# Kernel optimization log

Hardware: AMD Instinct MI355X
Metric: run time of the kernel (lower is better)

## Reference

```python
import jax, jax.numpy as jnp
import numpy as np
from jax import lax

NUM_DISP = 64
BLOCK = 21
EPS = 1e-12  # F.normalize default eps


def _box_sum(v):
    # v: (N, H, W) -> BLOCK x BLOCK zero-padded box sum (same shape), separable.
    p = BLOCK // 2
    v = v[:, None]  # (N,1,H,W)
    kv = jnp.ones((1, 1, BLOCK, 1), v.dtype)
    kh = jnp.ones((1, 1, 1, BLOCK), v.dtype)
    v = lax.conv_general_dilated(v, kv, (1, 1), ((p, p), (0, 0)))
    v = lax.conv_general_dilated(v, kh, (1, 1), ((0, 0), (p, p)))
    return v[:, 0]


def _l2norm_c(img):
    n = jnp.sqrt(jnp.sum(img * img, axis=1, keepdims=True))
    return img / jnp.maximum(n, EPS)


def _disparity(left, right):
    # left, right: (B, 3, H, W)
    left = _l2norm_c(left)
    right = _l2norm_c(right)
    B, C, H, W = left.shape
    d = jnp.arange(NUM_DISP)
    xs = jnp.arange(W)
    idx = xs[None, :] - d[:, None]              # (D, W): source column in right image
    valid = (idx >= 0)
    r_shift = right[:, :, :, jnp.clip(idx, 0)]  # (B, C, H, D, W)
    r_shift = jnp.where(valid[None, None, None], r_shift, 0.0)
    # per-pixel channel-summed absolute difference -> (B, D, H, W)
    diff = jnp.sum(jnp.abs(left[:, :, :, None, :] - r_shift), axis=1)  # (B, H, D, W)
    diff = jnp.transpose(diff, (0, 2, 1, 3))    # (B, D, H, W)
    cost = _box_sum(diff.reshape(B * NUM_DISP, H, W)).reshape(B, NUM_DISP, H, W)
    cost = cost / (C * BLOCK * BLOCK)           # mean SAD over block elements
    return jnp.argmin(cost, axis=1).astype(left.dtype)  # (B, H, W)


def setup_inputs() -> dict:
    key = jax.random.key(0)
    k1, k2 = jax.random.split(key)
    x = jax.random.normal(k1, (2, 6, 320, 512), dtype=jnp.float32)
    gt = jax.random.normal(k2, (2, 6, 320, 512), dtype=jnp.float32)
    return {"x": x, "gt": gt}


def reference(x, gt):
    disp_gt = _disparity(gt[:, :3], gt[:, 3:])
    disp_pred = _disparity(x[:, :3], x[:, 3:])
    return jnp.mean(jnp.abs(disp_pred - disp_gt))
```

## Files before the change

### kernel.cpp

```cpp
#include <hip/hip_runtime.h>
#include <math.h>

constexpr int B = 2, H = 320, W = 512, D = 64;
constexpr int HW = H * W;
constexpr int R = 10;
constexpr int SEG = 80;
constexpr int NSEG = H / SEG;
constexpr int RS = 548;
constexpr int QUADS = B * HW / 4;
constexpr float EPS = 1e-12f;
constexpr unsigned KM = 0xFFFFFFC0u;

__global__ void k_norm(const float* __restrict__ x, const float* __restrict__ gt,
                       float4* __restrict__ nrm4) {
    int idx = blockIdx.x * 128 + threadIdx.x;
    if (idx >= 2 * B * (HW / 4)) return;
    int t = idx / (B * (HW / 4));
    int rem = idx - t * (B * (HW / 4));
    int b = rem / (HW / 4);
    int hw4 = rem - b * (HW / 4);
    const float* p = (t == 0 ? x : gt) + (size_t)b * 6 * HW + 4 * hw4;
    float4 c[6];
#pragma unroll
    for (int ch = 0; ch < 6; ++ch) c[ch] = *(const float4*)(p + (size_t)ch * HW);
    float4* q = nrm4 + (size_t)(t * B + b) * 2 * HW + 4 * hw4;
    float4 o0[4], o1[4];
    const float* cf = (const float*)c;
#pragma unroll
    for (int k = 0; k < 4; ++k) {
        float v0 = cf[k], v1 = cf[4 + k], v2 = cf[8 + k];
        float v3 = cf[12 + k], v4 = cf[16 + k], v5 = cf[20 + k];
        float n1 = fmaxf(sqrtf(v0 * v0 + v1 * v1 + v2 * v2), EPS);
        float n2 = fmaxf(sqrtf(v3 * v3 + v4 * v4 + v5 * v5), EPS);
        o0[k] = make_float4(v0 / n1, v1 / n1, v2 / n1, 0.f);
        o1[k] = make_float4(v3 / n2, v4 / n2, v5 / n2, 0.f);
    }
#pragma unroll
    for (int k = 0; k < 4; ++k) { q[k] = o0[k]; q[HW + k] = o1[k]; }
}

template<bool FUSE>
__global__ __launch_bounds__(512, 2) void k_cost(const float4* __restrict__ nrm4,
                                                 float* __restrict__ cost,
                                                 const float* __restrict__ cprev,
                                                 float* __restrict__ dprev, int t) {
    const int blk = blockIdx.x;
    const int combo = blk & 7;
    const int d = blk >> 3;
    const int b = combo >> 2;
    const int seg = combo & 3;
    const int w = threadIdx.x;
    const float4* L4 = nrm4 + (size_t)(t * B + b) * 2 * HW;
    const float4* R4 = L4 + HW;
    const bool val = (w >= d);
    const int wr = val ? (w - d) : 0;
    const int h0 = seg * SEG;

    __shared__ float ring[21][W];
    __shared__ float vsb[2][8][RS];
    {
        int j = w >> 6, k = w & 63;
        if (k < 10)      { vsb[0][j][k] = 0.f;       vsb[1][j][k] = 0.f; }
        else if (k < 20) { vsb[0][j][512 + k] = 0.f; vsb[1][j][512 + k] = 0.f; }
    }

    auto diff = [&](int h) -> float {
        float4 l = L4[(size_t)h * W + w];
        if (val) {
            float4 r = R4[(size_t)h * W + wr];
            return fabsf(l.x - r.x) + fabsf(l.y - r.y) + fabsf(l.z - r.z);
        }
        return fabsf(l.x) + fabsf(l.y) + fabsf(l.z);
    };

    float vs = 0.f;
    for (int k = 0; k < 20; ++k) {
        int h = h0 - R + k;
        float dv0 = (h >= 0) ? diff(h) : 0.f;
        ring[k][w] = dv0;
        vs += dv0;
    }
    ring[20][w] = 0.f;

    const float* cp0 = nullptr; const float* cp1 = nullptr;
    int px0 = 0, px1 = 0;
    float best0 = 3.4e38f, best1 = 3.4e38f;
    int bd0 = 0, bd1 = 0;
    if (FUSE) {
        px0 = blk * 640 + w;
        int b0 = (px0 >= HW) ? 1 : 0;
        cp0 = cprev + (size_t)b0 * D * HW + (px0 - b0 * HW);
        if (w < 128) {
            px1 = blk * 640 + 512 + w;
            int b1 = (px1 >= HW) ? 1 : 0;
            cp1 = cprev + (size_t)b1 * D * HW + (px1 - b1 * HW);
        }
    }

    const int cc = threadIdx.x >> 3;
    const int jj = threadIdx.x & 7;
    float* cp = cost + ((size_t)(b * D + d) * H) * W;

    float dvv[8];
#pragma unroll
    for (int j = 0; j < 8; ++j) {
        int hn = h0 + j + R;
        dvv[j] = (hn < H) ? diff(hn) : 0.f;
    }

    int slot0 = 20;
    int dc = 0;
    for (int ss = 0; ss < 10; ++ss) {
        const int nd = (ss < 4) ? 7 : 6;
        int sl[8];
        float dold[8];
#pragma unroll
        for (int j = 0; j < 8; ++j) { int s2 = slot0 + j; if (s2 >= 21) s2 -= 21; sl[j] = s2; }
#pragma unroll
        for (int j = 0; j < 8; ++j) dold[j] = ring[sl[j]][w];
        float fv0[7], fv1[7];
        if (FUSE) {
#pragma unroll
            for (int q = 0; q < 7; ++q)
                if (q < nd) fv0[q] = cp0[(size_t)(dc + q) * HW];
            if (w < 128) {
#pragma unroll
                for (int q = 0; q < 7; ++q)
                    if (q < nd) fv1[q] = cp1[(size_t)(dc + q) * HW];
            }
        }
#pragma unroll
        for (int j = 0; j < 8; ++j) ring[sl[j]][w] = dvv[j];
        float* vrow = &vsb[ss & 1][0][0];
#pragma unroll
        for (int j = 0; j < 8; ++j) { vs += dvv[j] - dold[j]; vrow[j * RS + 10 + w] = vs; }
        float dvn[8];
        if (ss < 9) {
#pragma unroll
            for (int j = 0; j < 8; ++j) {
                int hn = h0 + (ss + 1) * 8 + j + R;
                dvn[j] = (hn < H) ? diff(hn) : 0.f;
            }
        } else {
#pragma unroll
            for (int j = 0; j < 8; ++j) dvn[j] = 0.f;
        }
        __syncthreads();
        const float* vp = &vsb[ss & 1][jj][8 * cc];
        float wnd[28];
#pragma unroll
        for (int q = 0; q < 7; ++q) {
            float4 v4 = *(const float4*)(vp + 4 * q);
            wnd[4 * q] = v4.x; wnd[4 * q + 1] = v4.y;
            wnd[4 * q + 2] = v4.z; wnd[4 * q + 3] = v4.w;
        }
        float o = 0.f;
#pragma unroll
        for (int k = 0; k < 21; ++k) o += wnd[k];
        float out[8];
        out[0] = o;
#pragma unroll
        for (int k = 1; k < 8; ++k) { o += wnd[20 + k] - wnd[k - 1]; out[k] = o; }
        float* op = cp + (size_t)(h0 + ss * 8 + jj) * W + 8 * cc;
        *(float4*)(op)     = make_float4(out[0], out[1], out[2], out[3]);
        *(float4*)(op + 4) = make_float4(out[4], out[5], out[6], out[7]);
        if (FUSE) {
#pragma unroll
            for (int q = 0; q < 7; ++q)
                if (q < nd && fv0[q] < best0) { best0 = fv0[q]; bd0 = dc + q; }
            if (w < 128) {
#pragma unroll
                for (int q = 0; q < 7; ++q)
                    if (q < nd && fv1[q] < best1) { best1 = fv1[q]; bd1 = dc + q; }
            }
        }
#pragma unroll
        for (int j = 0; j < 8; ++j) dvv[j] = dvn[j];
        dc += nd;
        slot0 += 8; if (slot0 >= 21) slot0 -= 21;
    }
    if (FUSE) {
        dprev[px0] = (float)bd0;
        if (w < 128) dprev[px1] = (float)bd1;
    }
}

__global__ void k_aminA(const float* __restrict__ cost, uint4* __restrict__ keys) {
    int idx = blockIdx.x * 256 + threadIdx.x;
    int c = idx / QUADS;
    int q = idx - c * QUADS;
    int b = q / (QUADS / B);
    int ql = q - b * (QUADS / B);
    const float* cp = cost + (size_t)b * D * HW + 4 * ql;
    int d0 = c * 16;
    float4 v = *(const float4*)(cp + (size_t)d0 * HW);
    unsigned kx = (__float_as_uint(v.x) & KM) | (unsigned)d0;
    unsigned ky = (__float_as_uint(v.y) & KM) | (unsigned)d0;
    unsigned kz = (__float_as_uint(v.z) & KM) | (unsigned)d0;
    unsigned kw = (__float_as_uint(v.w) & KM) | (unsigned)d0;
#pragma unroll 4
    for (int k = 1; k < 16; ++k) {
        unsigned d = (unsigned)(d0 + k);
        v = *(const float4*)(cp + (size_t)(d0 + k) * HW);
        unsigned e;
        e = (__float_as_uint(v.x) & KM) | d; kx = (e < kx) ? e : kx;
        e = (__float_as_uint(v.y) & KM) | d; ky = (e < ky) ? e : ky;
        e = (__float_as_uint(v.z) & KM) | d; kz = (e < kz) ? e : kz;
        e = (__float_as_uint(v.w) & KM) | d; kw = (e < kw) ? e : kw;
    }
    keys[idx] = make_uint4(kx, ky, kz, kw);
}

__global__ void k_aminB(const uint4* __restrict__ keys, const float* __restrict__ disp0,
                        float* __restrict__ part) {
    int q = blockIdx.x * 256 + threadIdx.x;
    uint4 m = keys[q];
#pragma unroll
    for (int c = 1; c < 4; ++c) {
        uint4 kc = keys[(size_t)c * QUADS + q];
        m.x = (kc.x < m.x) ? kc.x : m.x;
        m.y = (kc.y < m.y) ? kc.y : m.y;
        m.z = (kc.z < m.z) ? kc.z : m.z;
        m.w = (kc.w < m.w) ? kc.w : m.w;
    }
    float4 d0 = *(const float4*)(disp0 + (size_t)4 * q);
    float s = fabsf((float)(m.x & 63u) - d0.x) + fabsf((float)(m.y & 63u) - d0.y) +
              fabsf((float)(m.z & 63u) - d0.z) + fabsf((float)(m.w & 63u) - d0.w);
    __shared__ float sm[256];
    sm[threadIdx.x] = s;
    __syncthreads();
    for (int off = 128; off; off >>= 1) {
        if (threadIdx.x < off) sm[threadIdx.x] += sm[threadIdx.x + off];
        __syncthreads();
    }
    if (!threadIdx.x) part[blockIdx.x] = sm[0];
}

__global__ void k_amin(const float* __restrict__ cost, float* __restrict__ disp) {
    int blk = blockIdx.x;
    int b = (blk * 1024 >= HW) ? 1 : 0;
    int hw0 = blk * 1024 - b * HW + threadIdx.x * 4;
    const float* cp = cost + (size_t)b * D * HW + hw0;
    float4 v = *(const float4*)cp;
    float bb[4] = {v.x, v.y, v.z, v.w};
    int bd[4] = {0, 0, 0, 0};
    for (int d = 1; d < D; ++d) {
        v = *(const float4*)(cp + (size_t)d * HW);
        if (v.x < bb[0]) { bb[0] = v.x; bd[0] = d; }
        if (v.y < bb[1]) { bb[1] = v.y; bd[1] = d; }
        if (v.z < bb[2]) { bb[2] = v.z; bd[2] = d; }
        if (v.w < bb[3]) { bb[3] = v.w; bd[3] = d; }
    }
    *(float4*)(disp + (size_t)blk * 1024 + threadIdx.x * 4) =
        make_float4((float)bd[0], (float)bd[1], (float)bd[2], (float)bd[3]);
}

__global__ void k_red2(const float* __restrict__ part, float* __restrict__ out,
                       int nb, float inv) {
    __shared__ float sm[256];
    int tid = threadIdx.x;
    float s = 0.f;
    for (int i = tid; i < nb; i += 256) s += part[i];
    sm[tid] = s;
    __syncthreads();
    for (int off = 128; off; off >>= 1) {
        if (tid < off) sm[tid] += sm[tid + off];
        __syncthreads();
    }
    if (!tid) out[0] = sm[0] * inv;
}

extern "C" void kernel_launch(void* const* d_in, const int* in_sizes, int n_in,
                              void* d_out, int out_size, void* d_ws, size_t ws_size,
                              hipStream_t stream) {
    const float* x  = (const float*)d_in[0];
    const float* gt = (const float*)d_in[1];

    constexpr size_t NRM_F4 = (size_t)2 * B * 2 * HW;
    constexpr size_t COST_F = (size_t)B * D * HW;
    constexpr int NRM_BLKS  = (2 * B * (HW / 4) + 127) / 128;

    float4* nrm4 = (float4*)d_ws;
    float* cost0 = (float*)(nrm4 + NRM_F4);

    size_t need_primary = NRM_F4 * 16 + 2 * COST_F * 4 +
                          (size_t)4 * QUADS * 16 + (size_t)(B * HW + 4096) * 4;

    k_norm<<<NRM_BLKS, 128, 0, stream>>>(x, gt, nrm4);

    if (ws_size >= need_primary) {
        float* cost1 = cost0 + COST_F;
        uint4* kd    = (uint4*)(cost1 + COST_F);
        float* disp0 = (float*)(kd + (size_t)4 * QUADS);
        float* part  = disp0 + (size_t)B * HW;
        k_cost<false><<<B * NSEG * D, 512, 0, stream>>>(nrm4, cost0, nullptr, nullptr, 0);
        k_cost<true><<<B * NSEG * D, 512, 0, stream>>>(nrm4, cost1, cost0, disp0, 1);
        k_aminA<<<4 * QUADS / 256, 256, 0, stream>>>(cost1, kd);
        k_aminB<<<QUADS / 256, 256, 0, stream>>>(kd, disp0, part);
        k_red2<<<1, 256, 0, stream>>>(part, (float*)d_out, QUADS / 256, 1.f / (float)(B * HW));
    } else {
        float* disp0 = cost0 + COST_F;
        uint4* kd    = (uint4*)(disp0 + (size_t)B * HW);
        float* part  = (float*)(kd + (size_t)4 * QUADS);
        k_cost<false><<<B * NSEG * D, 512, 0, stream>>>(nrm4, cost0, nullptr, nullptr, 0);
        k_amin<<<B * HW / 1024, 256, 0, stream>>>(cost0, disp0);
        k_cost<false><<<B * NSEG * D, 512, 0, stream>>>(nrm4, cost0, nullptr, nullptr, 1);
        k_aminA<<<4 * QUADS / 256, 256, 0, stream>>>(cost0, kd);
        k_aminB<<<QUADS / 256, 256, 0, stream>>>(kd, disp0, part);
        k_red2<<<1, 256, 0, stream>>>(part, (float*)d_out, QUADS / 256, 1.f / (float)(B * HW));
    }
}
```

Before: 195.8 us.

## Tile cost volume as 8-row blocks with disparity-major inner layout

Changes the cost volume layout from (B,D,H,W) to (B, H/8, D, 8 rows, W), so each 8-row by 512-column tile for all disparities is contiguous. The producer kernel writes tiles and the argmin readers walk disparities with a fixed 4096-float stride inside one row-block. The goal is better DRAM page/TLB locality and L2 reuse when the argmin kernels and the fused pass read across disparities, at the cost of more complex indexing that has to be consistent across every kernel.

```diff
diff --git a/kernel.cpp b/kernel.cpp
--- a/kernel.cpp
+++ b/kernel.cpp
@@ -8,8 +8,13 @@
 constexpr int NSEG = H / SEG;
 constexpr int RS = 548;
 constexpr int QUADS = B * HW / 4;
+constexpr int NRB = H / 8;
 constexpr float EPS = 1e-12f;
 constexpr unsigned KM = 0xFFFFFFC0u;
+
+__device__ __forceinline__ size_t cbase(int b, int h, int w) {
+    return (((size_t)(b * NRB + (h >> 3)) * D) << 12) + ((size_t)(h & 7) << 9) + w;
+}
 
 __global__ void k_norm(const float* __restrict__ x, const float* __restrict__ gt,
                        float4* __restrict__ nrm4) {
@@ -82,24 +87,25 @@
     }
     ring[20][w] = 0.f;
 
-    const float* cp0 = nullptr; const float* cp1 = nullptr;
+    size_t base0 = 0, base1 = 0;
     int px0 = 0, px1 = 0;
     float best0 = 3.4e38f, best1 = 3.4e38f;
     int bd0 = 0, bd1 = 0;
     if (FUSE) {
         px0 = blk * 640 + w;
         int b0 = (px0 >= HW) ? 1 : 0;
-        cp0 = cprev + (size_t)b0 * D * HW + (px0 - b0 * HW);
+        int hw0 = px0 - b0 * HW;
+        base0 = cbase(b0, hw0 >> 9, hw0 & 511);
         if (w < 128) {
             px1 = blk * 640 + 512 + w;
             int b1 = (px1 >= HW) ? 1 : 0;
-            cp1 = cprev + (size_t)b1 * D * HW + (px1 - b1 * HW);
+            int hw1 = px1 - b1 * HW;
+            base1 = cbase(b1, hw1 >> 9, hw1 & 511);
         }
     }
 
     const int cc = threadIdx.x >> 3;
     const int jj = threadIdx.x & 7;
-    float* cp = cost + ((size_t)(b * D + d) * H) * W;
 
     float dvv[8];
 #pragma unroll
@@ -122,11 +128,11 @@
         if (FUSE) {
 #pragma unroll
             for (int q = 0; q < 7; ++q)
-                if (q < nd) fv0[q] = cp0[(size_t)(dc + q) * HW];
+                if (q < nd) fv0[q] = cprev[base0 + ((size_t)(dc + q) << 12)];
             if (w < 128) {
 #pragma unroll
                 for (int q = 0; q < 7; ++q)
-                    if (q < nd) fv1[q] = cp1[(size_t)(dc + q) * HW];
+                    if (q < nd) fv1[q] = cprev[base1 + ((size_t)(dc + q) << 12)];
             }
         }
 #pragma unroll
@@ -161,7 +167,8 @@
         out[0] = o;
 #pragma unroll
         for (int k = 1; k < 8; ++k) { o += wnd[20 + k] - wnd[k - 1]; out[k] = o; }
-        float* op = cp + (size_t)(h0 + ss * 8 + jj) * W + 8 * cc;
+        float* op = cost + (((size_t)(b * NRB + seg * 10 + ss) * D + d) << 12) +
+                    ((size_t)jj << 9) + 8 * cc;
         *(float4*)(op)     = make_float4(out[0], out[1], out[2], out[3]);
         *(float4*)(op + 4) = make_float4(out[4], out[5], out[6], out[7]);
         if (FUSE) {
@@ -191,9 +198,10 @@
     int q = idx - c * QUADS;
     int b = q / (QUADS / B);
     int ql = q - b * (QUADS / B);
-    const float* cp = cost + (size_t)b * D * HW + 4 * ql;
+    int hw = 4 * ql;
+    const float* cp = cost + cbase(b, hw >> 9, hw & 511);
     int d0 = c * 16;
-    float4 v = *(const float4*)(cp + (size_t)d0 * HW);
+    float4 v = *(const float4*)(cp + ((size_t)d0 << 12));
     unsigned kx = (__float_as_uint(v.x) & KM) | (unsigned)d0;
     unsigned ky = (__float_as_uint(v.y) & KM) | (unsigned)d0;
     unsigned kz = (__float_as_uint(v.z) & KM) | (unsigned)d0;
@@ -201,7 +209,7 @@
 #pragma unroll 4
     for (int k = 1; k < 16; ++k) {
         unsigned d = (unsigned)(d0 + k);
-        v = *(const float4*)(cp + (size_t)(d0 + k) * HW);
+        v = *(const float4*)(cp + ((size_t)(d0 + k) << 12));
         unsigned e;
         e = (__float_as_uint(v.x) & KM) | d; kx = (e < kx) ? e : kx;
         e = (__float_as_uint(v.y) & KM) | d; ky = (e < ky) ? e : ky;
@@ -237,21 +245,22 @@
 }
 
 __global__ void k_amin(const float* __restrict__ cost, float* __restrict__ disp) {
-    int blk = blockIdx.x;
-    int b = (blk * 1024 >= HW) ? 1 : 0;
-    int hw0 = blk * 1024 - b * HW + threadIdx.x * 4;
-    const float* cp = cost + (size_t)b * D * HW + hw0;
+    int idx = blockIdx.x * 256 + threadIdx.x;
+    int b = idx / (QUADS / B);
+    int ql = idx - b * (QUADS / B);
+    int hw = 4 * ql;
+    const float* cp = cost + cbase(b, hw >> 9, hw & 511);
     float4 v = *(const float4*)cp;
     float bb[4] = {v.x, v.y, v.z, v.w};
     int bd[4] = {0, 0, 0, 0};
     for (int d = 1; d < D; ++d) {
-        v = *(const float4*)(cp + (size_t)d * HW);
+        v = *(const float4*)(cp + ((size_t)d << 12));
         if (v.x < bb[0]) { bb[0] = v.x; bd[0] = d; }
         if (v.y < bb[1]) { bb[1] = v.y; bd[1] = d; }
         if (v.z < bb[2]) { bb[2] = v.z; bd[2] = d; }
         if (v.w < bb[3]) { bb[3] = v.w; bd[3] = d; }
     }
-    *(float4*)(disp + (size_t)blk * 1024 + threadIdx.x * 4) =
+    *(float4*)(disp + (size_t)4 * idx) =
         make_float4((float)bd[0], (float)bd[1], (float)bd[2], (float)bd[3]);
 }
 
@@ -303,7 +312,7 @@
         uint4* kd    = (uint4*)(disp0 + (size_t)B * HW);
         float* part  = (float*)(kd + (size_t)4 * QUADS);
         k_cost<false><<<B * NSEG * D, 512, 0, stream>>>(nrm4, cost0, nullptr, nullptr, 0);
-        k_amin<<<B * HW / 1024, 256, 0, stream>>>(cost0, disp0);
+        k_amin<<<QUADS / 256, 256, 0, stream>>>(cost0, disp0);
         k_cost<false><<<B * NSEG * D, 512, 0, stream>>>(nrm4, cost0, nullptr, nullptr, 1);
         k_aminA<<<4 * QUADS / 256, 256, 0, stream>>>(cost0, kd);
         k_aminB<<<QUADS / 256, 256, 0, stream>>>(kd, disp0, part);
```

Result: no change. 196.3 us (+0.3%).
